# Kernel optimization log

Hardware: AMD Instinct MI355X
Metric: run time of the kernel (lower is better)

Reference implementation:

```python
import jax, jax.numpy as jnp
import numpy as np

NCOLORS = 16      # distinct colors
NUM_DUPS = 4      # duplicates per color -> P = 64 blend points
N_VERTS = 5_000_000
R_THRESH = 0.3    # radius threshold
RAMP_SLOPE = 1.0  # blend ramp slope


def setup_inputs() -> dict:
    key = jax.random.key(0)
    k1, k2, k3 = jax.random.split(key, 3)
    P = NCOLORS * NUM_DUPS
    # spherical angles: theta in [0, pi], phi in [-pi, pi]
    u = jax.random.uniform(k1, (P, 2), dtype=jnp.float32)
    pointsSphere = jnp.stack([u[:, 0] * np.float32(np.pi),
                              (u[:, 1] * 2.0 - 1.0) * np.float32(np.pi)], axis=1)
    colors = jax.random.uniform(k2, (NCOLORS, 3), dtype=jnp.float32)
    v = jax.random.normal(k3, (N_VERTS, 3), dtype=jnp.float32)
    isoVert = v / jnp.linalg.norm(v, axis=1, keepdims=True)  # unit sphere verts
    return {"pointsSphere": pointsSphere, "colors": colors, "isoVert": isoVert}


def reference(pointsSphere, colors, isoVert):
    # spherical -> cartesian blend points, [P, 3]
    theta, phi = pointsSphere[:, 0], pointsSphere[:, 1]
    points = jnp.stack([jnp.sin(theta) * jnp.cos(phi),
                        jnp.sin(theta) * jnp.sin(phi),
                        jnp.cos(theta)], axis=1)
    P = points.shape[0]
    pcolors = colors[jnp.arange(P) % NCOLORS]  # color for each point, [P, 3]

    # Sequential blend over points (order matters), vectorized over all vertices.
    def step(c, pc):
        p, col = pc                                       # [3], [3]
        d = jnp.sqrt(jnp.sum((p[None, :] - isoVert) ** 2, axis=1))  # [N]
        blended = col[None, :] - (d * RAMP_SLOPE)[:, None] * (col[None, :] - c)
        c = jnp.where((d < R_THRESH)[:, None], blended, c)
        return c, None

    init = jnp.zeros_like(isoVert)  # [N, 3] vertex rgb, starts black
    verts_rgb, _ = jax.lax.scan(step, init, (points, pcolors))
    return verts_rgb
```

## Files before the change

### kernel.cpp

```cpp
#include <hip/hip_runtime.h>
#include <math.h>

#define S0_THRESH 0x1.70A3D8p-4f
#define DOT_HI 0.954989f

typedef float v2f __attribute__((ext_vector_type(2)));

__global__ void setup_points_kernel(const float* __restrict__ pointsSphere,
                                    const float* __restrict__ colors,
                                    float4* __restrict__ pc,
                                    int P, int ncolors) {
    int j = threadIdx.x;
    if (j >= P) return;
    double th = (double)pointsSphere[2 * j];
    double ph = (double)pointsSphere[2 * j + 1];
    float st = (float)sin(th);
    float ct = (float)cos(th);
    float sp = (float)sin(ph);
    float cp = (float)cos(ph);
    pc[2 * j] = make_float4(__fmul_rn(st, cp), __fmul_rn(st, sp), ct, 0.0f);
    const float* c = colors + 3 * (j % ncolors);
    pc[2 * j + 1] = make_float4(c[0], c[1], c[2], 0.0f);
}

__global__ __launch_bounds__(256, 8)
void blend_mask_kernel(const float* __restrict__ iso,
                       const float4* __restrict__ pc,
                       float* __restrict__ out,
                       int nverts) {
    __shared__ float4 spc[128];
    if (threadIdx.x < 128) spc[threadIdx.x] = pc[threadIdx.x];
    __syncthreads();

    int t = blockIdx.x * 256 + threadIdx.x;
    int i0 = 2 * t;
    if (i0 >= nverts) return;
    bool pair = (i0 + 1) < nverts;
    size_t base = 3 * (size_t)i0;

    v2f vvx, vvy, vvz;
    if (pair) {
        float2 a0 = *(const float2*)(iso + base);
        float2 a1 = *(const float2*)(iso + base + 2);
        float2 a2 = *(const float2*)(iso + base + 4);
        vvx = (v2f){a0.x, a1.y};
        vvy = (v2f){a0.y, a2.x};
        vvz = (v2f){a1.x, a2.y};
    } else {
        vvx = (v2f){iso[base], 0.0f};
        vvy = (v2f){iso[base + 1], 0.0f};
        vvz = (v2f){iso[base + 2], -2.0f};
    }

    unsigned lo0 = 0, hi0 = 0, lo1 = 0, hi1 = 0;
#pragma unroll 8
    for (int j = 63; j >= 32; --j) {
        float4 p = pc[2 * j];
        v2f acc = (v2f){p.z, p.z} * vvz;
        acc = __builtin_elementwise_fma((v2f){p.y, p.y}, vvy, acc);
        acc = __builtin_elementwise_fma((v2f){p.x, p.x}, vvx, acc);
        hi0 = (hi0 << 1) | (acc.x > DOT_HI ? 1u : 0u);
        hi1 = (hi1 << 1) | (acc.y > DOT_HI ? 1u : 0u);
    }
#pragma unroll 8
    for (int j = 31; j >= 0; --j) {
        float4 p = pc[2 * j];
        v2f acc = (v2f){p.z, p.z} * vvz;
        acc = __builtin_elementwise_fma((v2f){p.y, p.y}, vvy, acc);
        acc = __builtin_elementwise_fma((v2f){p.x, p.x}, vvx, acc);
        lo0 = (lo0 << 1) | (acc.x > DOT_HI ? 1u : 0u);
        lo1 = (lo1 << 1) | (acc.y > DOT_HI ? 1u : 0u);
    }

    float cx0 = 0.f, cy0 = 0.f, cz0 = 0.f;
    float cx1 = 0.f, cy1 = 0.f, cz1 = 0.f;

    auto resolve32 = [&](unsigned m, int jbase, float vx, float vy, float vz,
                         float& cx, float& cy, float& cz) {
        while (m) {
            int j = jbase + __builtin_ctz(m);
            m &= m - 1;
            float4 p   = spc[2 * j];
            float4 col = spc[2 * j + 1];
            float dx = __fsub_rn(p.x, vx);
            float dy = __fsub_rn(p.y, vy);
            float dz = __fsub_rn(p.z, vz);
            float s = __fadd_rn(__fadd_rn(__fmul_rn(dx, dx), __fmul_rn(dy, dy)),
                                __fmul_rn(dz, dz));
            if (s < S0_THRESH) {
                float d = __builtin_amdgcn_sqrtf(s);
                cx = fmaf(-d, __fsub_rn(col.x, cx), col.x);
                cy = fmaf(-d, __fsub_rn(col.y, cy), col.y);
                cz = fmaf(-d, __fsub_rn(col.z, cz), col.z);
            }
        }
    };

    resolve32(lo0,  0, vvx.x, vvy.x, vvz.x, cx0, cy0, cz0);
    resolve32(hi0, 32, vvx.x, vvy.x, vvz.x, cx0, cy0, cz0);
    resolve32(lo1,  0, vvx.y, vvy.y, vvz.y, cx1, cy1, cz1);
    resolve32(hi1, 32, vvx.y, vvy.y, vvz.y, cx1, cy1, cz1);

    if (pair) {
        *(float2*)(out + base)     = make_float2(cx0, cy0);
        *(float2*)(out + base + 2) = make_float2(cz0, cx1);
        *(float2*)(out + base + 4) = make_float2(cy1, cz1);
    } else {
        out[base] = cx0; out[base + 1] = cy0; out[base + 2] = cz0;
    }
}

extern "C" void kernel_launch(void* const* d_in, const int* in_sizes, int n_in,
                              void* d_out, int out_size, void* d_ws, size_t ws_size,
                              hipStream_t stream) {
    const float* pointsSphere = (const float*)d_in[0];
    const float* colors       = (const float*)d_in[1];
    const float* iso          = (const float*)d_in[2];
    int P       = in_sizes[0] / 2;
    int ncolors = in_sizes[1] / 3;
    int nverts  = in_sizes[2] / 3;

    float4* pc = (float4*)d_ws;

    hipLaunchKernelGGL(setup_points_kernel, dim3(1), dim3(64), 0, stream,
                       pointsSphere, colors, pc, P, ncolors);

    int nthreads = (nverts + 1) / 2;
    int blocks = (nthreads + 255) / 256;
    hipLaunchKernelGGL(blend_mask_kernel, dim3(blocks), dim3(256), 0, stream,
                       iso, pc, (float*)d_out, nverts);
}
```

Baseline: 155.4 us.

## Bin blend points into a 3D grid of per-cell candidate lists

Adds a kernel that builds, for each cell of a 16^3 grid over [-1,1]^3, a byte list of blend points within a conservative radius of the cell centre. The main kernel then looks up its vertex's cell and tests only those candidates instead of dot-testing all 64 points. The aim is to remove most of the per-vertex 64-point culling pass. In exchange it adds an extra launch, a scattered list load per vertex, and scalar one-vertex-per-thread loads and stores in place of the paired float2 accesses. Divergent loop lengths across lanes are another risk. It falls back to the old kernel if the workspace is too small.

```diff
diff --git a/kernel.cpp b/kernel.cpp
--- a/kernel.cpp
+++ b/kernel.cpp
@@ -3,6 +3,11 @@
 
 #define S0_THRESH 0x1.70A3D8p-4f
 #define DOT_HI 0.954989f
+
+#define NCELL 16
+#define CELL_STRIDE 32
+#define LIST_BYTES (4096 * CELL_STRIDE)
+#define LIST_R2 0.1681
 
 typedef float v2f __attribute__((ext_vector_type(2)));
 
@@ -21,6 +26,89 @@
     pc[2 * j] = make_float4(__fmul_rn(st, cp), __fmul_rn(st, sp), ct, 0.0f);
     const float* c = colors + 3 * (j % ncolors);
     pc[2 * j + 1] = make_float4(c[0], c[1], c[2], 0.0f);
+}
+
+__global__ void build_lists_kernel(const float4* __restrict__ pc,
+                                   unsigned char* __restrict__ lists) {
+    int cell = blockIdx.x * 256 + threadIdx.x;
+    if (cell >= 4096) return;
+    int cx = cell & 15, cy = (cell >> 4) & 15, cz = cell >> 8;
+    double ccx = -1.0 + (cx + 0.5) * 0.125;
+    double ccy = -1.0 + (cy + 0.5) * 0.125;
+    double ccz = -1.0 + (cz + 0.5) * 0.125;
+    unsigned char* L = lists + (size_t)cell * CELL_STRIDE;
+    int n = 0;
+    bool ovf = false;
+    for (int j = 0; j < 64; ++j) {
+        float4 p = pc[2 * j];
+        double dx = (double)p.x - ccx;
+        double dy = (double)p.y - ccy;
+        double dz = (double)p.z - ccz;
+        if (dx * dx + dy * dy + dz * dz <= LIST_R2) {
+            if (n < 31) { L[1 + n] = (unsigned char)j; ++n; }
+            else ovf = true;
+        }
+    }
+    L[0] = ovf ? 0xFFu : (unsigned char)n;
+}
+
+__global__ __launch_bounds__(256, 8)
+void blend_cell_kernel(const float* __restrict__ iso,
+                       const float4* __restrict__ pc,
+                       const unsigned char* __restrict__ lists,
+                       float* __restrict__ out,
+                       int nverts) {
+    __shared__ float4 spc[128];
+    if (threadIdx.x < 128) spc[threadIdx.x] = pc[threadIdx.x];
+    __syncthreads();
+
+    int i = blockIdx.x * 256 + threadIdx.x;
+    if (i >= nverts) return;
+    size_t base = 3 * (size_t)i;
+    float vx = iso[base], vy = iso[base + 1], vz = iso[base + 2];
+
+    int cxi = (int)((vx + 1.0f) * 8.0f); cxi = cxi > 15 ? 15 : cxi;
+    int cyi = (int)((vy + 1.0f) * 8.0f); cyi = cyi > 15 ? 15 : cyi;
+    int czi = (int)((vz + 1.0f) * 8.0f); czi = czi > 15 ? 15 : czi;
+    int cell = (czi << 8) | (cyi << 4) | cxi;
+
+    const unsigned char* L = lists + (size_t)cell * CELL_STRIDE;
+    unsigned long long w = *(const unsigned long long*)L;
+    int count = (int)(w & 0xFFull);
+
+    float cxc = 0.f, cyc = 0.f, czc = 0.f;
+
+    auto resolve = [&](int j) {
+        float4 p   = spc[2 * j];
+        float4 col = spc[2 * j + 1];
+        float dx = __fsub_rn(p.x, vx);
+        float dy = __fsub_rn(p.y, vy);
+        float dz = __fsub_rn(p.z, vz);
+        float s = __fadd_rn(__fadd_rn(__fmul_rn(dx, dx), __fmul_rn(dy, dy)),
+                            __fmul_rn(dz, dz));
+        if (s < S0_THRESH) {
+            float d = __builtin_amdgcn_sqrtf(s);
+            cxc = fmaf(-d, __fsub_rn(col.x, cxc), col.x);
+            cyc = fmaf(-d, __fsub_rn(col.y, cyc), col.y);
+            czc = fmaf(-d, __fsub_rn(col.z, czc), col.z);
+        }
+    };
+
+    if (count == 0xFF) {
+        for (int j = 0; j < 64; ++j) resolve(j);
+    } else {
+        unsigned long long bits = w >> 8;
+        for (int k = 0; k < count; ++k) {
+            if (k == 7)       bits = *(const unsigned long long*)(L + 8);
+            else if (k == 15) bits = *(const unsigned long long*)(L + 16);
+            else if (k == 23) bits = *(const unsigned long long*)(L + 24);
+            int j = (int)(bits & 0xFFull);
+            bits >>= 8;
+            resolve(j);
+        }
+    }
+
+    out[base] = cxc; out[base + 1] = cyc; out[base + 2] = czc;
 }
 
 __global__ __launch_bounds__(256, 8)
@@ -121,12 +209,21 @@
     int nverts  = in_sizes[2] / 3;
 
     float4* pc = (float4*)d_ws;
+    unsigned char* lists = (unsigned char*)d_ws + 2048;
 
     hipLaunchKernelGGL(setup_points_kernel, dim3(1), dim3(64), 0, stream,
                        pointsSphere, colors, pc, P, ncolors);
 
-    int nthreads = (nverts + 1) / 2;
-    int blocks = (nthreads + 255) / 256;
-    hipLaunchKernelGGL(blend_mask_kernel, dim3(blocks), dim3(256), 0, stream,
-                       iso, pc, (float*)d_out, nverts);
-}
+    if (ws_size >= 2048 + LIST_BYTES) {
+        hipLaunchKernelGGL(build_lists_kernel, dim3(16), dim3(256), 0, stream,
+                           pc, lists);
+        int blocks = (nverts + 255) / 256;
+        hipLaunchKernelGGL(blend_cell_kernel, dim3(blocks), dim3(256), 0, stream,
+                           iso, pc, lists, (float*)d_out, nverts);
+    } else {
+        int nthreads = (nverts + 1) / 2;
+        int blocks = (nthreads + 255) / 256;
+        hipLaunchKernelGGL(blend_mask_kernel, dim3(blocks), dim3(256), 0, stream,
+                           iso, pc, (float*)d_out, nverts);
+    }
+}
```

Result: no change. 156.3 us (+0.5%).
